# Performance work log

Measured on AMD Instinct MI355X. Metric: run time of the kernel, lower is better.

## Reference

```python
import jax, jax.numpy as jnp
import numpy as np

N_NODES = 50000
N_EDGES = 800000
IN_DIM = 768
HID = 32
HEADS = 4
OUT_DIM = 128


def setup_inputs() -> dict:
    key = jax.random.key(0)
    ks = jax.random.split(key, 7)
    h = jax.random.normal(ks[0], (N_NODES, IN_DIM), dtype=jnp.float32)
    W1 = jax.random.normal(ks[1], (HEADS, IN_DIM, HID), dtype=jnp.float32) * (1.0 / np.sqrt(IN_DIM))
    a1 = jax.random.normal(ks[2], (HEADS, 2 * HID), dtype=jnp.float32) * (1.0 / np.sqrt(2 * HID))
    W2 = jax.random.normal(ks[3], (1, HEADS * HID, OUT_DIM), dtype=jnp.float32) * (1.0 / np.sqrt(HEADS * HID))
    a2 = jax.random.normal(ks[4], (1, 2 * OUT_DIM), dtype=jnp.float32) * (1.0 / np.sqrt(2 * OUT_DIM))
    src = jax.random.randint(ks[5], (N_EDGES,), 0, N_NODES, dtype=jnp.int32)
    dst = jax.random.randint(ks[6], (N_EDGES,), 0, N_NODES, dtype=jnp.int32)
    return {"h": h, "W1": W1, "a1": a1, "W2": W2, "a2": a2, "src": src, "dst": dst}


def gat_layer(h, W, a, src, dst, n_nodes):
    # W: [H, Din, D], a: [H, 2D]; returns concat of heads: [N, H*D]
    z = jnp.einsum('ni,hio->nho', h, W)          # [N, H, D]
    D = z.shape[-1]
    a_src, a_dst = a[:, :D], a[:, D:]
    s_src = jnp.einsum('nhd,hd->nh', z, a_src)   # [N, H]
    s_dst = jnp.einsum('nhd,hd->nh', z, a_dst)
    e = jax.nn.leaky_relu(s_src[src] + s_dst[dst], 0.01)  # [E, H]
    # edge softmax over incoming edges of each dst node
    e_max = jax.ops.segment_max(e, dst, num_segments=n_nodes)
    e_max = jnp.where(jnp.isfinite(e_max), e_max, 0.0)     # empty segments -> -inf
    ex = jnp.exp(e - e_max[dst])
    denom = jax.ops.segment_sum(ex, dst, num_segments=n_nodes)
    alpha = ex / jnp.maximum(denom[dst], 1e-9)             # [E, H]
    msg = alpha[:, :, None] * z[src]                       # [E, H, D]
    out = jax.ops.segment_sum(msg, dst, num_segments=n_nodes)  # [N, H, D]
    return out.reshape(n_nodes, -1)


def reference(h, W1, a1, W2, a2, src, dst):
    n = h.shape[0]
    h1 = jax.nn.elu(gat_layer(h, W1, a1, src, dst, n))   # [N, HEADS*HID]
    h2 = gat_layer(h1, W2, a2, src, dst, n)              # [N, OUT_DIM]
    return h2
```

## Files before the change

kernel.cpp:

```cpp
#include <hip/hip_runtime.h>

#define NN 50000
#define NE 800000
#define IND 768
#define CH  128
#define NBLK 196
#define GBM 64
#define GBK 32
#define MBLKS 782

typedef __attribute__((ext_vector_type(8))) short bf16x8;
typedef __attribute__((ext_vector_type(4))) float f32x4;

__device__ __forceinline__ unsigned short bf16_rne(float f) {
    unsigned u = __float_as_uint(f);
    u += 0x7fffu + ((u >> 16) & 1u);
    return (unsigned short)(u >> 16);
}
__device__ __forceinline__ float bf16_to_f(unsigned short b) {
    return __uint_as_float(((unsigned)b) << 16);
}

__device__ __forceinline__ void cvt_split_pk(const float4& u0, const float4& u1,
                                             uint4& hi, uint4& lo)
{
    unsigned h0, h1, h2, h3;
    asm("v_cvt_pk_bf16_f32 %0, %1, %2" : "=v"(h0) : "v"(u0.x), "v"(u0.y));
    asm("v_cvt_pk_bf16_f32 %0, %1, %2" : "=v"(h1) : "v"(u0.z), "v"(u0.w));
    asm("v_cvt_pk_bf16_f32 %0, %1, %2" : "=v"(h2) : "v"(u1.x), "v"(u1.y));
    asm("v_cvt_pk_bf16_f32 %0, %1, %2" : "=v"(h3) : "v"(u1.z), "v"(u1.w));
    const float l0 = u0.x - __uint_as_float(h0 << 16);
    const float l1 = u0.y - __uint_as_float(h0 & 0xffff0000u);
    const float l2 = u0.z - __uint_as_float(h1 << 16);
    const float l3 = u0.w - __uint_as_float(h1 & 0xffff0000u);
    const float l4 = u1.x - __uint_as_float(h2 << 16);
    const float l5 = u1.y - __uint_as_float(h2 & 0xffff0000u);
    const float l6 = u1.z - __uint_as_float(h3 << 16);
    const float l7 = u1.w - __uint_as_float(h3 & 0xffff0000u);
    unsigned g0, g1, g2, g3;
    asm("v_cvt_pk_bf16_f32 %0, %1, %2" : "=v"(g0) : "v"(l0), "v"(l1));
    asm("v_cvt_pk_bf16_f32 %0, %1, %2" : "=v"(g1) : "v"(l2), "v"(l3));
    asm("v_cvt_pk_bf16_f32 %0, %1, %2" : "=v"(g2) : "v"(l4), "v"(l5));
    asm("v_cvt_pk_bf16_f32 %0, %1, %2" : "=v"(g3) : "v"(l6), "v"(l7));
    hi = make_uint4(h0, h1, h2, h3);
    lo = make_uint4(g0, g1, g2, g3);
}

__global__ void prep_b1(const float* __restrict__ W1,
                        unsigned short* __restrict__ Bhi, unsigned short* __restrict__ Blo)
{
    int idx = blockIdx.x * blockDim.x + threadIdx.x;
    if (idx >= CH * IND) return;
    int n = idx / IND, k = idx % IND;
    float v = W1[(size_t)(n >> 5) * IND * 32 + (size_t)k * 32 + (n & 31)];
    int kt = k >> 5, kk = k & 31, j = kk >> 3, e = kk & 7;
    int g = n * 4 + (j ^ ((n >> 1) & 3));
    int off = kt * 4096 + g * 8 + e;
    unsigned short hi = bf16_rne(v);
    float lo = v - bf16_to_f(hi);
    Bhi[off] = hi;
    Blo[off] = bf16_rne(lo);
}

__global__ void prep_b2(const float* __restrict__ W2,
                        unsigned short* __restrict__ Bhi, unsigned short* __restrict__ Blo)
{
    int idx = blockIdx.x * blockDim.x + threadIdx.x;
    if (idx >= CH * CH) return;
    int n = idx / CH, k = idx % CH;
    float v = W2[(size_t)k * CH + n];
    int kt = k >> 5, kk = k & 31, j = kk >> 3, e = kk & 7;
    int g = n * 4 + (j ^ ((n >> 1) & 3));
    int off = kt * 4096 + g * 8 + e;
    unsigned short hi = bf16_rne(v);
    float lo = v - bf16_to_f(hi);
    Bhi[off] = hi;
    Blo[off] = bf16_rne(lo);
}

template<int H>
__global__ __launch_bounds__(256) void gemm_fused(
    const float* __restrict__ A,
    const unsigned short* __restrict__ Bthi, const unsigned short* __restrict__ Btlo,
    const float* __restrict__ av,
    unsigned short* __restrict__ Z16,
    float* __restrict__ ss, float* __restrict__ sd, int K)
{
    __shared__ unsigned short Ahi[2048];
    __shared__ unsigned short Alo[2048];
    __shared__ unsigned short Bs[2][4096];
    __shared__ float sred[2][64][2];

    const int t = threadIdx.x;
    const int lane = t & 63;
    const int w = t >> 6;
    const int wr = w >> 1, wc = w & 1;
    const int lrow = lane & 15, kg = lane >> 4;
    const int m0 = blockIdx.x * GBM;
    const int nt = K >> 5;

    const int ar = t >> 2, aj = t & 3;
    const bool avalid = (m0 + ar) < NN;
    const float* aptr = A + (size_t)(avalid ? (m0 + ar) : 0) * K + aj * 8;
    const int ag8 = (ar * 4 + (aj ^ ((ar >> 1) & 3))) * 8;

    int aoff[2];
    #pragma unroll
    for (int mi = 0; mi < 2; ++mi) {
        const int r = wr * 32 + mi * 16 + lrow;
        aoff[mi] = (r * 4 + (kg ^ ((r >> 1) & 3))) * 8;
    }
    int boff[4];
    #pragma unroll
    for (int ni = 0; ni < 4; ++ni) {
        const int n = wc * 64 + ni * 16 + lrow;
        boff[ni] = (n * 4 + (kg ^ ((n >> 1) & 3))) * 8;
    }

    f32x4 acc[2][4];
    #pragma unroll
    for (int i = 0; i < 2; ++i)
        #pragma unroll
        for (int j = 0; j < 4; ++j) acc[i][j] = (f32x4)(0.f);

    for (int kt = 0; kt < nt; ++kt) {
        float4 v0 = make_float4(0.f, 0.f, 0.f, 0.f);
        float4 v1 = make_float4(0.f, 0.f, 0.f, 0.f);
        if (avalid) {
            const float* p = aptr + kt * GBK;
            v0 = *(const float4*)p;
            v1 = *(const float4*)(p + 4);
        }
        uint4 hi, lo;
        cvt_split_pk(v0, v1, hi, lo);
        __syncthreads();
        *(uint4*)&Ahi[ag8] = hi;
        *(uint4*)&Alo[ag8] = lo;
        #pragma unroll
        for (int i = 0; i < 4; ++i) {
            const int c = w * 4 + i;
            const int plane = c >> 3;
            const int co = (c & 7) * 512;
            const unsigned short* gs =
                (plane ? Btlo : Bthi) + (size_t)kt * 4096 + co + lane * 8;
            __builtin_amdgcn_global_load_lds(
                (const __attribute__((address_space(1))) unsigned int*)gs,
                (__attribute__((address_space(3))) unsigned int*)&Bs[plane][co],
                16, 0, 0);
        }
        __syncthreads();

        bf16x8 ahi[2], alo[2];
        #pragma unroll
        for (int mi = 0; mi < 2; ++mi) {
            ahi[mi] = *(const bf16x8*)&Ahi[aoff[mi]];
            alo[mi] = *(const bf16x8*)&Alo[aoff[mi]];
        }
        #pragma unroll
        for (int ni = 0; ni < 4; ++ni) {
            const bf16x8 bhi = *(const bf16x8*)&Bs[0][boff[ni]];
            const bf16x8 blo = *(const bf16x8*)&Bs[1][boff[ni]];
            #pragma unroll
            for (int mi = 0; mi < 2; ++mi) {
                acc[mi][ni] = __builtin_amdgcn_mfma_f32_16x16x32_bf16(ahi[mi], bhi, acc[mi][ni], 0, 0, 0);
                acc[mi][ni] = __builtin_amdgcn_mfma_f32_16x16x32_bf16(ahi[mi], blo, acc[mi][ni], 0, 0, 0);
                acc[mi][ni] = __builtin_amdgcn_mfma_f32_16x16x32_bf16(alo[mi], bhi, acc[mi][ni], 0, 0, 0);
            }
        }
    }

    const int NH = (H == 4) ? 2 : 1;
    float asc[4], adc[4];
    #pragma unroll
    for (int ni = 0; ni < 4; ++ni) {
        const int col = wc * 64 + ni * 16 + lrow;
        if (H == 4) {
            const int hh = col >> 5, d = col & 31;
            asc[ni] = av[hh * 64 + d];
            adc[ni] = av[hh * 64 + 32 + d];
        } else {
            asc[ni] = av[col];
            adc[ni] = av[128 + col];
        }
    }
    float es[2][4][2], ed[2][4][2];
    #pragma unroll
    for (int mi = 0; mi < 2; ++mi)
        #pragma unroll
        for (int j = 0; j < 4; ++j)
            #pragma unroll
            for (int q = 0; q < 2; ++q) { es[mi][j][q] = 0.f; ed[mi][j][q] = 0.f; }

    #pragma unroll
    for (int mi = 0; mi < 2; ++mi) {
        #pragma unroll
        for (int ni = 0; ni < 4; ++ni) {
            const int hh = (H == 4) ? (ni >> 1) : 0;
            const f32x4 a = acc[mi][ni];
            #pragma unroll
            for (int j = 0; j < 4; ++j) {
                es[mi][j][hh] = fmaf(a[j], asc[ni], es[mi][j][hh]);
                ed[mi][j][hh] = fmaf(a[j], adc[ni], ed[mi][j][hh]);
            }
        }
    }
    #pragma unroll
    for (int mi = 0; mi < 2; ++mi) {
        const int rbase = m0 + wr * 32 + mi * 16 + kg * 4;
        #pragma unroll
        for (int ni = 0; ni < 4; ++ni) {
            const int col = wc * 64 + ni * 16 + lrow;
            const f32x4 a = acc[mi][ni];
            #pragma unroll
            for (int j = 0; j < 4; ++j) {
                const int r = rbase + j;
                if (r < NN) Z16[(size_t)r * CH + col] = bf16_rne(a[j]);
            }
        }
    }
    #pragma unroll
    for (int off = 1; off < 16; off <<= 1) {
        #pragma unroll
        for (int mi = 0; mi < 2; ++mi)
            #pragma unroll
            for (int j = 0; j < 4; ++j)
                #pragma unroll
                for (int q = 0; q < NH; ++q) {
                    es[mi][j][q] += __shfl_xor(es[mi][j][q], off, 64);
                    ed[mi][j][q] += __shfl_xor(ed[mi][j][q], off, 64);
                }
    }
    if (H == 4) {
        if (lrow == 0) {
            #pragma unroll
            for (int mi = 0; mi < 2; ++mi)
                #pragma unroll
                for (int j = 0; j < 4; ++j) {
                    const int r = m0 + wr * 32 + mi * 16 + kg * 4 + j;
                    if (r < NN) {
                        #pragma unroll
                        for (int q = 0; q < 2; ++q) {
                            ss[r * 4 + wc * 2 + q] = es[mi][j][q];
                            sd[r * 4 + wc * 2 + q] = ed[mi][j][q];
                        }
                    }
                }
        }
    } else {
        if (lrow == 0) {
            #pragma unroll
            for (int mi = 0; mi < 2; ++mi)
                #pragma unroll
                for (int j = 0; j < 4; ++j) {
                    const int rl = wr * 32 + mi * 16 + kg * 4 + j;
                    sred[0][rl][wc] = es[mi][j][0];
                    sred[1][rl][wc] = ed[mi][j][0];
                }
        }
        __syncthreads();
        if (t < 64) {
            const int r = m0 + t;
            if (r < NN) {
                ss[r] = sred[0][t][0] + sred[0][t][1];
                sd[r] = sred[1][t][0] + sred[1][t][1];
            }
        }
    }
}

__global__ __launch_bounds__(256) void zero_cc(int* __restrict__ counts, int* __restrict__ cursor)
{
    int i = blockIdx.x * 256 + threadIdx.x;
    if (i < NN) { counts[i] = 0; cursor[i] = 0; }
}

__global__ void count_k(const int* __restrict__ dst, int* __restrict__ counts)
{
    int e = blockIdx.x * blockDim.x + threadIdx.x;
    if (e < NE) atomicAdd(&counts[dst[e]], 1);
}

__global__ __launch_bounds__(256) void scan1(const int* __restrict__ counts,
                                             int* __restrict__ exc, int* __restrict__ bsum)
{
    __shared__ int s[256];
    const int t = threadIdx.x;
    const int i = blockIdx.x * 256 + t;
    const int val = (i < NN) ? counts[i] : 0;
    s[t] = val;
    __syncthreads();
    #pragma unroll
    for (int off = 1; off < 256; off <<= 1) {
        int v = (t >= off) ? s[t - off] : 0;
        __syncthreads();
        s[t] += v;
        __syncthreads();
    }
    if (i < NN) exc[i] = s[t] - val;
    if (t == 255) bsum[blockIdx.x] = s[255];
}

__global__ __launch_bounds__(256) void scan2(const int* __restrict__ bsum,
                                             int* __restrict__ bexc)
{
    __shared__ int s[256];
    const int t = threadIdx.x;
    const int val = (t < NBLK) ? bsum[t] : 0;
    s[t] = val;
    __syncthreads();
    #pragma unroll
    for (int off = 1; off < 256; off <<= 1) {
        int v = (t >= off) ? s[t - off] : 0;
        __syncthreads();
        s[t] += v;
        __syncthreads();
    }
    bexc[t] = s[t] - val;
}

__global__ __launch_bounds__(256) void scan3(const int* __restrict__ exc,
                                             const int* __restrict__ bexc,
                                             int* __restrict__ offsets)
{
    const int i = blockIdx.x * 256 + threadIdx.x;
    if (i < NN) offsets[i] = exc[i] + bexc[i >> 8];
    if (i == 0) offsets[NN] = NE;
}

__global__ void scatter_es(const int* __restrict__ src, const int* __restrict__ dst,
                           const int* __restrict__ offsets, int* __restrict__ cursor,
                           int* __restrict__ es)
{
    int e = blockIdx.x * blockDim.x + threadIdx.x;
    if (e >= NE) return;
    int d = dst[e];
    int p = offsets[d] + atomicAdd(&cursor[d], 1);
    es[p] = src[e];
}

template<int H, bool ELU>
__global__ __launch_bounds__(256) void fused_agg(
    const int* __restrict__ offsets, const int* __restrict__ es,
    const float* __restrict__ s_src, const float* __restrict__ s_dst,
    const unsigned short* __restrict__ z16, float* __restrict__ out)
{
    const int wid = threadIdx.x >> 6;
    const int lane = threadIdx.x & 63;
    const int n = blockIdx.x * 4 + wid;
    const int beg = offsets[n], end = offsets[n + 1];
    const int deg = end - beg;

    __shared__ float alpha_sh[4][128][H];
    __shared__ int   es_sh[4][128];
    __shared__ int   maxdeg;
    if (threadIdx.x == 0) maxdeg = 0;
    __syncthreads();
    if (lane == 0) atomicMax(&maxdeg, deg);
    __syncthreads();

    float sdv[H];
    #pragma unroll
    for (int h = 0; h < H; ++h) sdv[h] = s_dst[(size_t)n * H + h];

    const int myh = (H == 4) ? (lane >> 4) : 0;
    float m[H], ssum[H], inv[H];
    #pragma unroll
    for (int h = 0; h < H; ++h) { m[h] = -INFINITY; ssum[h] = 0.f; }
    float2 acc = make_float2(0.f, 0.f);

    if (maxdeg <= 128) {
        for (int idx = lane; idx < deg; idx += 64) {
            const int s = es[beg + idx];
            es_sh[wid][idx] = s;
            if (H == 4) {
                const float4 sv = *(const float4*)&s_src[(size_t)s * 4];
                const float svv[4] = {sv.x, sv.y, sv.z, sv.w};
                float v4[4];
                #pragma unroll
                for (int h = 0; h < 4; ++h) {
                    float v = svv[h] + sdv[h];
                    v = v > 0.f ? v : 0.01f * v;
                    v4[h] = v;
                    const float mn = fmaxf(m[h], v);
                    ssum[h] = ssum[h] * __expf(m[h] - mn) + __expf(v - mn);
                    m[h] = mn;
                }
                *(float4*)&alpha_sh[wid][idx][0] = make_float4(v4[0], v4[1], v4[2], v4[3]);
            } else {
                float v = s_src[s] + sdv[0];
                v = v > 0.f ? v : 0.01f * v;
                alpha_sh[wid][idx][0] = v;
                const float mn = fmaxf(m[0], v);
                ssum[0] = ssum[0] * __expf(m[0] - mn) + __expf(v - mn);
                m[0] = mn;
            }
        }
        #pragma unroll
        for (int h = 0; h < H; ++h) {
            float mg = m[h];
            #pragma unroll
            for (int off = 1; off < 64; off <<= 1)
                mg = fmaxf(mg, __shfl_xor(mg, off, 64));
            float sg = ssum[h] * __expf(m[h] - mg);
            #pragma unroll
            for (int off = 1; off < 64; off <<= 1)
                sg += __shfl_xor(sg, off, 64);
            m[h] = mg;
            inv[h] = 1.0f / fmaxf(sg, 1e-9f);
        }
        for (int idx = lane; idx < deg; idx += 64) {
            #pragma unroll
            for (int h = 0; h < H; ++h)
                alpha_sh[wid][idx][h] = __expf(alpha_sh[wid][idx][h] - m[h]) * inv[h];
        }
        int j = 0;
        for (; j + 4 <= deg; j += 4) {
            const int s0 = es_sh[wid][j],     s1 = es_sh[wid][j + 1];
            const int s2 = es_sh[wid][j + 2], s3 = es_sh[wid][j + 3];
            const float a0 = alpha_sh[wid][j][myh],     a1 = alpha_sh[wid][j + 1][myh];
            const float a2 = alpha_sh[wid][j + 2][myh], a3 = alpha_sh[wid][j + 3][myh];
            const ushort2 u0 = *(const ushort2*)&z16[(size_t)s0 * CH + lane * 2];
            const ushort2 u1 = *(const ushort2*)&z16[(size_t)s1 * CH + lane * 2];
            const ushort2 u2 = *(const ushort2*)&z16[(size_t)s2 * CH + lane * 2];
            const ushort2 u3 = *(const ushort2*)&z16[(size_t)s3 * CH + lane * 2];
            acc.x = fmaf(a0, bf16_to_f(u0.x), acc.x); acc.y = fmaf(a0, bf16_to_f(u0.y), acc.y);
            acc.x = fmaf(a1, bf16_to_f(u1.x), acc.x); acc.y = fmaf(a1, bf16_to_f(u1.y), acc.y);
            acc.x = fmaf(a2, bf16_to_f(u2.x), acc.x); acc.y = fmaf(a2, bf16_to_f(u2.y), acc.y);
            acc.x = fmaf(a3, bf16_to_f(u3.x), acc.x); acc.y = fmaf(a3, bf16_to_f(u3.y), acc.y);
        }
        for (; j < deg; ++j) {
            const int s0 = es_sh[wid][j];
            const float a0 = alpha_sh[wid][j][myh];
            const ushort2 u0 = *(const ushort2*)&z16[(size_t)s0 * CH + lane * 2];
            acc.x = fmaf(a0, bf16_to_f(u0.x), acc.x); acc.y = fmaf(a0, bf16_to_f(u0.y), acc.y);
        }
    } else {
        const int nch = (maxdeg + 127) >> 7;
        for (int i = beg + lane; i < end; i += 64) {
            const int s = es[i];
            if (H == 4) {
                const float4 sv = *(const float4*)&s_src[(size_t)s * 4];
                const float svv[4] = {sv.x, sv.y, sv.z, sv.w};
                #pragma unroll
                for (int h = 0; h < 4; ++h) {
                    float v = svv[h] + sdv[h];
                    v = v > 0.f ? v : 0.01f * v;
                    const float mn = fmaxf(m[h], v);
                    ssum[h] = ssum[h] * __expf(m[h] - mn) + __expf(v - mn);
                    m[h] = mn;
                }
            } else {
                float v = s_src[s] + sdv[0];
                v = v > 0.f ? v : 0.01f * v;
                const float mn = fmaxf(m[0], v);
                ssum[0] = ssum[0] * __expf(m[0] - mn) + __expf(v - mn);
                m[0] = mn;
            }
        }
        #pragma unroll
        for (int h = 0; h < H; ++h) {
            float mg = m[h];
            #pragma unroll
            for (int off = 1; off < 64; off <<= 1)
                mg = fmaxf(mg, __shfl_xor(mg, off, 64));
            float sg = ssum[h] * __expf(m[h] - mg);
            #pragma unroll
            for (int off = 1; off < 64; off <<= 1)
                sg += __shfl_xor(sg, off, 64);
            m[h] = mg;
            inv[h] = 1.0f / fmaxf(sg, 1e-9f);
        }
        for (int k = 0; k < nch; ++k) {
            const int base = beg + k * 128;
            int cnt = end - base;
            cnt = cnt < 0 ? 0 : (cnt > 128 ? 128 : cnt);
            for (int idx = lane; idx < cnt; idx += 64) {
                const int s = es[base + idx];
                es_sh[wid][idx] = s;
                if (H == 4) {
                    const float4 sv = *(const float4*)&s_src[(size_t)s * 4];
                    const float svv[4] = {sv.x, sv.y, sv.z, sv.w};
                    float a4[4];
                    #pragma unroll
                    for (int h = 0; h < 4; ++h) {
                        float v = svv[h] + sdv[h];
                        v = v > 0.f ? v : 0.01f * v;
                        a4[h] = __expf(v - m[h]) * inv[h];
                    }
                    *(float4*)&alpha_sh[wid][idx][0] = make_float4(a4[0], a4[1], a4[2], a4[3]);
                } else {
                    float v = s_src[s] + sdv[0];
                    v = v > 0.f ? v : 0.01f * v;
                    alpha_sh[wid][idx][0] = __expf(v - m[0]) * inv[0];
                }
            }
            __syncthreads();
            for (int j = 0; j < cnt; ++j) {
                const int s0 = es_sh[wid][j];
                const float a0 = alpha_sh[wid][j][myh];
                const ushort2 u0 = *(const ushort2*)&z16[(size_t)s0 * CH + lane * 2];
                acc.x = fmaf(a0, bf16_to_f(u0.x), acc.x);
                acc.y = fmaf(a0, bf16_to_f(u0.y), acc.y);
            }
            __syncthreads();
        }
    }

    if (ELU) {
        acc.x = acc.x > 0.f ? acc.x : expm1f(acc.x);
        acc.y = acc.y > 0.f ? acc.y : expm1f(acc.y);
    }
    *(float2*)&out[(size_t)n * CH + lane * 2] = acc;
}

extern "C" void kernel_launch(void* const* d_in, const int* in_sizes, int n_in,
                              void* d_out, int out_size, void* d_ws, size_t ws_size,
                              hipStream_t stream)
{
    const float* h   = (const float*)d_in[0];
    const float* W1  = (const float*)d_in[1];
    const float* a1  = (const float*)d_in[2];
    const float* W2  = (const float*)d_in[3];
    const float* a2  = (const float*)d_in[4];
    const int*   src = (const int*)d_in[5];
    const int*   dst = (const int*)d_in[6];
    float* out = (float*)d_out;

    char* ws = (char*)d_ws;
    unsigned short* Bthi1 = (unsigned short*)(ws + 0);
    unsigned short* Btlo1 = (unsigned short*)(ws + 196608);
    unsigned short* Bthi2 = (unsigned short*)(ws + 393216);
    unsigned short* Btlo2 = (unsigned short*)(ws + 425984);
    float* ss      = (float*)(ws + 458752);
    float* sd      = (float*)(ws + 1258752);
    int*   counts  = (int*)  (ws + 2058752);
    int*   exc     = (int*)  (ws + 2258752);
    int*   bsum    = (int*)  (ws + 2458752);
    int*   bexc    = (int*)  (ws + 2459776);
    int*   offsets = (int*)  (ws + 2460800);
    int*   cursor  = (int*)  (ws + 2661056);
    int*   es      = (int*)  (ws + 2861056);
    unsigned short* z16 = (unsigned short*)(ws + 6061056);
    float* h1      = (float*)(ws + 18861056);

    const int EB = 256;
    const int egrid = (NE + EB - 1) / EB;
    const int sgrid = NN / 4;

    zero_cc<<<NBLK, 256, 0, stream>>>(counts, cursor);
    count_k<<<egrid, EB, 0, stream>>>(dst, counts);
    scan1<<<NBLK, 256, 0, stream>>>(counts, exc, bsum);
    scan2<<<1, 256, 0, stream>>>(bsum, bexc);
    scan3<<<NBLK, 256, 0, stream>>>(exc, bexc, offsets);
    scatter_es<<<egrid, EB, 0, stream>>>(src, dst, offsets, cursor, es);

    prep_b1<<<(CH * IND + 255) / 256, 256, 0, stream>>>(W1, Bthi1, Btlo1);
    prep_b2<<<(CH * CH + 255) / 256, 256, 0, stream>>>(W2, Bthi2, Btlo2);

    gemm_fused<4><<<MBLKS, 256, 0, stream>>>(h, Bthi1, Btlo1, a1, z16, ss, sd, IND);
    fused_agg<4, true><<<sgrid, 256, 0, stream>>>(offsets, es, ss, sd, z16, h1);

    gemm_fused<1><<<MBLKS, 256, 0, stream>>>(h1, Bthi2, Btlo2, a2, z16, ss, sd, CH);
    fused_agg<1, false><<<sgrid, 256, 0, stream>>>(offsets, es, ss, sd, z16, out);
}
```

Before: 245.3 us.

## Double GEMM K-step to 64 and make aggregation degree branching per-wave

The fused GEMM now stages two 32-wide K sub-tiles of A and B into shared memory per iteration. This halves the number of block barriers and global-to-LDS rounds across the K loop, at the cost of double the LDS footprint. The aggregation kernel drops the block-wide max-degree reduction and its barriers, so each wave picks the short or chunked path from its own node's degree. It also removes the block barriers in the chunked path, relying on each wave touching only its own shared slices. The risk is a hidden barrier inside the per-wave branch, or ordering issues once the barriers are gone.

Measured after the change: 250.2 us. Within noise of the previous version (+2.0%).

```diff
diff --git a/kernel.cpp b/kernel.cpp
--- a/kernel.cpp
+++ b/kernel.cpp
@@ -6,7 +6,6 @@
 #define CH  128
 #define NBLK 196
 #define GBM 64
-#define GBK 32
 #define MBLKS 782
 
 typedef __attribute__((ext_vector_type(8))) short bf16x8;
@@ -86,9 +85,9 @@
     unsigned short* __restrict__ Z16,
     float* __restrict__ ss, float* __restrict__ sd, int K)
 {
-    __shared__ unsigned short Ahi[2048];
-    __shared__ unsigned short Alo[2048];
-    __shared__ unsigned short Bs[2][4096];
+    __shared__ unsigned short Ahi[2][2048];
+    __shared__ unsigned short Alo[2][2048];
+    __shared__ unsigned short Bs[2][2][4096];
     __shared__ float sred[2][64][2];
 
     const int t = threadIdx.x;
@@ -97,7 +96,7 @@
     const int wr = w >> 1, wc = w & 1;
     const int lrow = lane & 15, kg = lane >> 4;
     const int m0 = blockIdx.x * GBM;
-    const int nt = K >> 5;
+    const int nt = K >> 6;
 
     const int ar = t >> 2, aj = t & 3;
     const bool avalid = (m0 + ar) < NN;
@@ -124,47 +123,57 @@
         for (int j = 0; j < 4; ++j) acc[i][j] = (f32x4)(0.f);
 
     for (int kt = 0; kt < nt; ++kt) {
-        float4 v0 = make_float4(0.f, 0.f, 0.f, 0.f);
-        float4 v1 = make_float4(0.f, 0.f, 0.f, 0.f);
+        float4 v00 = make_float4(0.f, 0.f, 0.f, 0.f), v01 = v00, v10 = v00, v11 = v00;
         if (avalid) {
-            const float* p = aptr + kt * GBK;
-            v0 = *(const float4*)p;
-            v1 = *(const float4*)(p + 4);
-        }
-        uint4 hi, lo;
-        cvt_split_pk(v0, v1, hi, lo);
-        __syncthreads();
-        *(uint4*)&Ahi[ag8] = hi;
-        *(uint4*)&Alo[ag8] = lo;
-        #pragma unroll
-        for (int i = 0; i < 4; ++i) {
-            const int c = w * 4 + i;
-            const int plane = c >> 3;
-            const int co = (c & 7) * 512;
-            const unsigned short* gs =
-                (plane ? Btlo : Bthi) + (size_t)kt * 4096 + co + lane * 8;
-            __builtin_amdgcn_global_load_lds(
-                (const __attribute__((address_space(1))) unsigned int*)gs,
-                (__attribute__((address_space(3))) unsigned int*)&Bs[plane][co],
-                16, 0, 0);
-        }
-        __syncthreads();
-
-        bf16x8 ahi[2], alo[2];
-        #pragma unroll
-        for (int mi = 0; mi < 2; ++mi) {
-            ahi[mi] = *(const bf16x8*)&Ahi[aoff[mi]];
-            alo[mi] = *(const bf16x8*)&Alo[aoff[mi]];
-        }
-        #pragma unroll
-        for (int ni = 0; ni < 4; ++ni) {
-            const bf16x8 bhi = *(const bf16x8*)&Bs[0][boff[ni]];
-            const bf16x8 blo = *(const bf16x8*)&Bs[1][boff[ni]];
+            const float* p = aptr + kt * 64;
+            v00 = *(const float4*)p;        v01 = *(const float4*)(p + 4);
+            v10 = *(const float4*)(p + 32); v11 = *(const float4*)(p + 36);
+        }
+        __syncthreads();
+        {
+            uint4 hi, lo;
+            cvt_split_pk(v00, v01, hi, lo);
+            *(uint4*)&Ahi[0][ag8] = hi;
+            *(uint4*)&Alo[0][ag8] = lo;
+            cvt_split_pk(v10, v11, hi, lo);
+            *(uint4*)&Ahi[1][ag8] = hi;
+            *(uint4*)&Alo[1][ag8] = lo;
+        }
+        #pragma unroll
+        for (int sub = 0; sub < 2; ++sub) {
+            #pragma unroll
+            for (int i = 0; i < 4; ++i) {
+                const int c = w * 4 + i;
+                const int plane = c >> 3;
+                const int co = (c & 7) * 512;
+                const unsigned short* gs =
+                    (plane ? Btlo : Bthi) + (size_t)(kt * 2 + sub) * 4096 + co + lane * 8;
+                __builtin_amdgcn_global_load_lds(
+                    (const __attribute__((address_space(1))) unsigned int*)gs,
+                    (__attribute__((address_space(3))) unsigned int*)&Bs[sub][plane][co],
+                    16, 0, 0);
+            }
+        }
+        __syncthreads();
+
+        #pragma unroll
+        for (int sub = 0; sub < 2; ++sub) {
+            bf16x8 ahi[2], alo[2];
             #pragma unroll
             for (int mi = 0; mi < 2; ++mi) {
-                acc[mi][ni] = __builtin_amdgcn_mfma_f32_16x16x32_bf16(ahi[mi], bhi, acc[mi][ni], 0, 0, 0);
-                acc[mi][ni] = __builtin_amdgcn_mfma_f32_16x16x32_bf16(ahi[mi], blo, acc[mi][ni], 0, 0, 0);
-                acc[mi][ni] = __builtin_amdgcn_mfma_f32_16x16x32_bf16(alo[mi], bhi, acc[mi][ni], 0, 0, 0);
+                ahi[mi] = *(const bf16x8*)&Ahi[sub][aoff[mi]];
+                alo[mi] = *(const bf16x8*)&Alo[sub][aoff[mi]];
+            }
+            #pragma unroll
+            for (int ni = 0; ni < 4; ++ni) {
+                const bf16x8 bhi = *(const bf16x8*)&Bs[sub][0][boff[ni]];
+                const bf16x8 blo = *(const bf16x8*)&Bs[sub][1][boff[ni]];
+                #pragma unroll
+                for (int mi = 0; mi < 2; ++mi) {
+                    acc[mi][ni] = __builtin_amdgcn_mfma_f32_16x16x32_bf16(ahi[mi], bhi, acc[mi][ni], 0, 0, 0);
+                    acc[mi][ni] = __builtin_amdgcn_mfma_f32_16x16x32_bf16(ahi[mi], blo, acc[mi][ni], 0, 0, 0);
+                    acc[mi][ni] = __builtin_amdgcn_mfma_f32_16x16x32_bf16(alo[mi], bhi, acc[mi][ni], 0, 0, 0);
+                }
             }
         }
     }
@@ -352,11 +361,6 @@
 
     __shared__ float alpha_sh[4][128][H];
     __shared__ int   es_sh[4][128];
-    __shared__ int   maxdeg;
-    if (threadIdx.x == 0) maxdeg = 0;
-    __syncthreads();
-    if (lane == 0) atomicMax(&maxdeg, deg);
-    __syncthreads();
 
     float sdv[H];
     #pragma unroll
@@ -368,7 +372,7 @@
     for (int h = 0; h < H; ++h) { m[h] = -INFINITY; ssum[h] = 0.f; }
     float2 acc = make_float2(0.f, 0.f);
 
-    if (maxdeg <= 128) {
+    if (deg <= 128) {
         for (int idx = lane; idx < deg; idx += 64) {
             const int s = es[beg + idx];
             es_sh[wid][idx] = s;
@@ -435,7 +439,6 @@
             acc.x = fmaf(a0, bf16_to_f(u0.x), acc.x); acc.y = fmaf(a0, bf16_to_f(u0.y), acc.y);
         }
     } else {
-        const int nch = (maxdeg + 127) >> 7;
         for (int i = beg + lane; i < end; i += 64) {
             const int s = es[i];
             if (H == 4) {
@@ -470,6 +473,7 @@
             m[h] = mg;
             inv[h] = 1.0f / fmaxf(sg, 1e-9f);
         }
+        const int nch = (deg + 127) >> 7;
         for (int k = 0; k < nch; ++k) {
             const int base = beg + k * 128;
             int cnt = end - base;
@@ -494,7 +498,6 @@
                     alpha_sh[wid][idx][0] = __expf(v - m[0]) * inv[0];
                 }
             }
-            __syncthreads();
             for (int j = 0; j < cnt; ++j) {
                 const int s0 = es_sh[wid][j];
                 const float a0 = alpha_sh[wid][j][myh];
@@ -502,7 +505,6 @@
                 acc.x = fmaf(a0, bf16_to_f(u0.x), acc.x);
                 acc.y = fmaf(a0, bf16_to_f(u0.y), acc.y);
             }
-            __syncthreads();
         }
     }
 
```
